# Performance work log

Measured on AMD Instinct MI355X. Metric: run time of the kernel, lower is better.

The kernel has to match this reference:

```python
import jax, jax.numpy as jnp
import numpy as np

N_NODES = 50000
N_EDGES = 800000
D_IN = 128
D_OUT = 128


def setup_inputs() -> dict:
    key = jax.random.key(0)
    k1, k2, k3, k4, k5 = jax.random.split(key, 5)
    x = jax.random.normal(k1, (N_NODES, D_IN), dtype=jnp.float32)
    edge_index = jax.random.randint(k2, (2, N_EDGES), 0, N_NODES, dtype=jnp.int64)
    # PyG SAGEConv params: lin_l (neighbors, with bias), lin_r (root, no bias)
    scale = 1.0 / np.sqrt(D_IN)
    W_l = jax.random.uniform(k3, (D_OUT, D_IN), dtype=jnp.float32, minval=-scale, maxval=scale)
    b_l = jax.random.uniform(k4, (D_OUT,), dtype=jnp.float32, minval=-scale, maxval=scale)
    W_r = jax.random.uniform(k5, (D_OUT, D_IN), dtype=jnp.float32, minval=-scale, maxval=scale)
    return {"x": x, "edge_index": edge_index, "W_l": W_l, "b_l": b_l, "W_r": W_r}


def reference(x, edge_index, W_l, b_l, W_r):
    src, dst = edge_index[0], edge_index[1]
    # mean aggregation of neighbor (source) features into destination nodes
    msg = x[src]  # [E, D_IN]
    agg_sum = jax.ops.segment_sum(msg, dst, num_segments=N_NODES)  # [N, D_IN]
    deg = jax.ops.segment_sum(jnp.ones((N_EDGES,), dtype=x.dtype), dst, num_segments=N_NODES)
    agg = agg_sum / jnp.maximum(deg, 1.0)[:, None]  # isolated nodes -> 0
    # out = lin_l(agg) + lin_r(x); ReLU from SAGE_NET wrapper (active=True)
    out = agg @ W_l.T + b_l + x @ W_r.T
    return jax.nn.relu(out)
```

## Files before the change

kernel.cpp:

```cpp
#include <hip/hip_runtime.h>
#include <hip/hip_bf16.h>

#define NNODES 50000
#define NEDGES 800000
#define DD 128
#define NPART 8
#define PSIZE 6250
#define CAP 64
#define NGROUPS 3910
#define WK_B (NGROUPS * 8 + 64)
#define WP2 68
#define ZROW ((u32)NNODES)

typedef unsigned int u32;
typedef unsigned short u16;
typedef short bf16x8 __attribute__((ext_vector_type(8)));
typedef float f32x4 __attribute__((ext_vector_type(4)));
typedef float f32x2 __attribute__((ext_vector_type(2)));

#if defined(__has_builtin)
#if __has_builtin(__builtin_amdgcn_cvt_pk_f32_fp8)
#define HAVE_HW_FP8 1
#endif
#endif

union U4B8 {
    uint4 u;
    bf16x8 b;
};

__device__ __forceinline__ u32 f2b(float f) {
    u32 u = __float_as_uint(f);
    u32 rounding = 0x7fffu + ((u >> 16) & 1u);
    return (u + rounding) >> 16;
}

__device__ __forceinline__ u32 f2e4m3(float f) {
    u32 u = __float_as_uint(f);
    u32 s = (u >> 31) << 7;
    u32 mag = u & 0x7fffffffu;
    if (mag < 0x3c800000u) return s;
    u32 t = mag + 0x0007FFFFu + ((mag >> 20) & 1u);
    u32 e = (t >> 23) - 120u;
    u32 m = (t >> 20) & 7u;
    if (e > 15u || (e == 15u && m == 7u)) { e = 15u; m = 6u; }
    return s | (e << 3) | m;
}

__device__ __forceinline__ void fp8x4_acc(u32 v, float& a0, float& a1,
                                          float& a2, float& a3) {
#ifdef HAVE_HW_FP8
    f32x2 lo = __builtin_amdgcn_cvt_pk_f32_fp8((int)v, false);
    f32x2 hi = __builtin_amdgcn_cvt_pk_f32_fp8((int)v, true);
    a0 += lo.x;
    a1 += lo.y;
    a2 += hi.x;
    a3 += hi.y;
#else
#pragma unroll
    for (int b = 0; b < 4; ++b) {
        u32 byte = (v >> (8 * b)) & 0xffu;
        u32 f = ((byte >> 7) << 31) | ((((byte >> 3) & 15u) + 120u) << 23) |
                ((byte & 7u) << 20);
        float val = (byte & 0x78u) ? __uint_as_float(f) : 0.f;
        if (b == 0) a0 += val;
        else if (b == 1) a1 += val;
        else if (b == 2) a2 += val;
        else a3 += val;
    }
#endif
}

__global__ __launch_bounds__(256) void work_k(
    const int* __restrict__ ei, u32* __restrict__ deg,
    u16* __restrict__ slots16, const float* __restrict__ x,
    u32* __restrict__ xb, u32* __restrict__ xq,
    const float* __restrict__ Wl, const float* __restrict__ Wr,
    u32* __restrict__ wb) {
    const int b = blockIdx.x, tid = threadIdx.x;
    if (b < NGROUPS * 8) {
        const u32 g = (u32)b >> 3, r8 = (u32)b & 7u;
        const u32 gm = g % 5u, gq = g / 5u;
        if (gm < 4u) {
            u32 fg = gq * 4u + gm;
            if (fg < 3125u) {
                u32 e = fg * 256u + tid;
                int dst = ei[NEDGES + e];
                if ((u32)(dst - r8 * PSIZE) < (u32)PSIZE) {
                    u32 pos = atomicAdd(deg + dst, 1u);
                    if (pos < CAP) slots16[(size_t)dst * CAP + pos] = (u16)ei[e];
                }
            }
        } else {
            u32 xi = gq * 8u + r8;
            if (xi < 6250u) {
                int i = (int)xi * 256 + tid;
                float4 v = ((const float4*)x)[i];
                uint2 o;
                o.x = f2b(v.x) | (f2b(v.y) << 16);
                o.y = f2b(v.z) | (f2b(v.w) << 16);
                ((uint2*)xb)[i] = o;
                xq[i] = f2e4m3(v.x) | (f2e4m3(v.y) << 8) | (f2e4m3(v.z) << 16) |
                        (f2e4m3(v.w) << 24);
            }
        }
    } else {
        int idx = (b - NGROUPS * 8) * 256 + tid;
        int o = idx >> 7, c = idx & 127, k0 = 2 * c;
        const float* src = (k0 < DD) ? (Wl + o * DD + k0) : (Wr + o * DD + (k0 - DD));
        wb[idx] = f2b(src[0]) | (f2b(src[1]) << 16);
        if (b == WK_B - 1 && tid < 32)
            xq[(size_t)ZROW * 32 + tid] = 0u;
    }
}

__global__ __launch_bounds__(256) void gather_k(
    const u32* __restrict__ xq, const u16* __restrict__ slots16,
    const u32* __restrict__ deg, u32* __restrict__ aggb) {
    u32 gid = blockIdx.x * 256u + threadIdx.x;
    u32 node = gid >> 6;
    u32 lane = gid & 63u;
    if (node >= NNODES) return;
    u32 d = deg[node];
    u32 cnt = min(d, (u32)CAP);
    u32 svp = (lane < cnt) ? (u32)slots16[(size_t)node * CAP + lane] : ZROW;
    const u32 half = lane >> 5;
    const u32 q = lane & 31u;
    float a0 = 0.f, a1 = 0.f, a2 = 0.f, a3 = 0.f;
    for (u32 j = 0; j < cnt; j += 16) {
        u32 v[8];
#pragma unroll
        for (int p = 0; p < 8; ++p) {
            u32 sA = __shfl(svp, (int)(j + 2 * p), 64);
            u32 sB = __shfl(svp, (int)(j + 2 * p + 1), 64);
            u32 s = half ? sB : sA;
            v[p] = xq[(size_t)s * 32 + q];
        }
#pragma unroll
        for (int p = 0; p < 8; ++p) fp8x4_acc(v[p], a0, a1, a2, a3);
    }
    a0 += __shfl_xor(a0, 32, 64);
    a1 += __shfl_xor(a1, 32, 64);
    a2 += __shfl_xor(a2, 32, 64);
    a3 += __shfl_xor(a3, 32, 64);
    if (lane < 32) {
        float inv = 1.0f / fmaxf((float)d, 1.0f);
        uint2 o;
        o.x = f2b(a0 * inv) | (f2b(a1 * inv) << 16);
        o.y = f2b(a2 * inv) | (f2b(a3 * inv) << 16);
        *(uint2*)&aggb[(size_t)node * 64 + q * 2] = o;
    }
}

__global__ __launch_bounds__(512, 4) void gemm_k(
    const u32* __restrict__ aggb, const u32* __restrict__ xb,
    const u32* __restrict__ wb, const float* __restrict__ bl,
    float* __restrict__ out) {
    __shared__ u32 w2[DD * WP2];
    __shared__ float sbias[DD];
    const int tid = threadIdx.x;
    const int row0 = blockIdx.x * 64;
    const int wave = tid >> 6, lane = tid & 63;
    const int m = lane & 15, quad = lane >> 4;
    const int rw = wave & 3;
    const int ch = wave >> 2;

    uint4 af_a[4], af_x[4];
    {
        int r = row0 + rw * 16 + m;
        r = r < NNODES ? r : NNODES - 1;
        const u32* arow = aggb + (size_t)r * 64;
        const u32* xrow = xb + (size_t)r * 64;
#pragma unroll
        for (int ks = 0; ks < 4; ++ks) {
            af_a[ks] = *(const uint4*)&arow[ks * 16 + quad * 4];
            af_x[ks] = *(const uint4*)&xrow[ks * 16 + quad * 4];
        }
    }

    for (int r = tid >> 5; r < DD; r += 16) {
        int c2 = (tid & 31) * 2;
        *(uint2*)&w2[r * WP2 + c2] = *(const uint2*)&wb[r * DD + c2];
    }
    if (tid < DD) sbias[tid] = bl[tid];
    __syncthreads();

    f32x4 acc[4];
#pragma unroll
    for (int nt = 0; nt < 4; ++nt) acc[nt] = (f32x4){0.f, 0.f, 0.f, 0.f};

#pragma unroll
    for (int ks = 0; ks < 4; ++ks) {
        U4B8 af;
        af.u = af_a[ks];
#pragma unroll
        for (int nt = 0; nt < 4; ++nt) {
            U4B8 bf;
            bf.u = *(const uint4*)&w2[((ch * 4 + nt) * 16 + m) * WP2 + ks * 16 +
                                      quad * 4];
            acc[nt] = __builtin_amdgcn_mfma_f32_16x16x32_bf16(af.b, bf.b,
                                                              acc[nt], 0, 0, 0);
        }
    }
    __syncthreads();
    for (int r = tid >> 5; r < DD; r += 16) {
        int c2 = (tid & 31) * 2;
        *(uint2*)&w2[r * WP2 + c2] = *(const uint2*)&wb[r * DD + 64 + c2];
    }
    __syncthreads();

#pragma unroll
    for (int ks = 0; ks < 4; ++ks) {
        U4B8 af;
        af.u = af_x[ks];
#pragma unroll
        for (int nt = 0; nt < 4; ++nt) {
            U4B8 bf;
            bf.u = *(const uint4*)&w2[((ch * 4 + nt) * 16 + m) * WP2 + ks * 16 +
                                      quad * 4];
            acc[nt] = __builtin_amdgcn_mfma_f32_16x16x32_bf16(af.b, bf.b,
                                                              acc[nt], 0, 0, 0);
        }
    }

#pragma unroll
    for (int nt = 0; nt < 4; ++nt) {
        int col = (ch * 4 + nt) * 16 + m;
        float b = sbias[col];
#pragma unroll
        for (int r_ = 0; r_ < 4; ++r_) {
            int row = row0 + rw * 16 + quad * 4 + r_;
            if (row < NNODES)
                out[(size_t)row * DD + col] = fmaxf(acc[nt][r_] + b, 0.f);
        }
    }
}

__global__ __launch_bounds__(256) void scatter_k(
    const float* __restrict__ x, const int* __restrict__ ei,
    float* __restrict__ agg, u32* __restrict__ deg) {
    u32 gid = blockIdx.x * 256u + threadIdx.x;
    u32 edge = gid >> 6;
    u32 lane = gid & 63u;
    if (edge >= NEDGES) return;
    int src = ei[edge];
    int dst = ei[NEDGES + edge];
    float2 v = ((const float2*)(x + (size_t)src * DD))[lane];
    float* p = agg + (size_t)dst * DD + lane * 2u;
    unsafeAtomicAdd(p, v.x);
    unsafeAtomicAdd(p + 1, v.y);
    if (lane == 0) atomicAdd(deg + dst, 1u);
}

__global__ __launch_bounds__(256) void mean_k(
    float* __restrict__ agg, const u32* __restrict__ deg) {
    u32 gid = blockIdx.x * 256u + threadIdx.x;
    u32 node = gid >> 6;
    u32 lane = gid & 63u;
    if (node >= NNODES) return;
    float inv = 1.0f / fmaxf((float)deg[node], 1.0f);
    float2* p = (float2*)(agg + (size_t)node * DD) + lane;
    float2 v = *p;
    *p = make_float2(v.x * inv, v.y * inv);
}

__global__ __launch_bounds__(256) void lin_l_k(
    float* __restrict__ agg,
    const float* __restrict__ Wl, const float* __restrict__ bl) {
    __shared__ u32 WT[DD * 65];
    __shared__ float rows[4 * DD];
    __shared__ float sbias[DD];
    const int tid = threadIdx.x;
    {
        u16* WTs = (u16*)WT;
        for (int i = tid; i < DD * DD; i += 256) {
            int o = i >> 7, k = i & 127;
            WTs[k * 130 + o] = (u16)f2b(Wl[i]);
        }
        if (tid < DD) sbias[tid] = bl[tid];
    }
    __syncthreads();
    const int h = tid & 63;
    const int nl = tid >> 6;
    for (int base = blockIdx.x * 4; base < NNODES; base += gridDim.x * 4) {
        ((float2*)rows)[tid] =
            ((const float2*)(agg + (size_t)(base + (tid >> 6)) * DD))[tid & 63];
        __syncthreads();
        float acc0 = sbias[2 * h], acc1 = sbias[2 * h + 1];
#pragma unroll
        for (int k = 0; k < DD; ++k) {
            float a = rows[nl * DD + k];
            u32 w2 = WT[k * 65 + h];
            acc0 = fmaf(a, __uint_as_float(w2 << 16), acc0);
            acc1 = fmaf(a, __uint_as_float(w2 & 0xffff0000u), acc1);
        }
        __syncthreads();
        ((float2*)(agg + (size_t)(base + nl) * DD))[h] = make_float2(acc0, acc1);
    }
}

__global__ __launch_bounds__(256) void lin_r_k(
    float* __restrict__ io, const float* __restrict__ x,
    const float* __restrict__ Wr) {
    __shared__ u32 WT[DD * 65];
    __shared__ float rows[4 * DD];
    const int tid = threadIdx.x;
    {
        u16* WTs = (u16*)WT;
        for (int i = tid; i < DD * DD; i += 256) {
            int o = i >> 7, k = i & 127;
            WTs[k * 130 + o] = (u16)f2b(Wr[i]);
        }
    }
    __syncthreads();
    const int h = tid & 63;
    const int nl = tid >> 6;
    for (int base = blockIdx.x * 4; base < NNODES; base += gridDim.x * 4) {
        ((float2*)rows)[tid] =
            ((const float2*)(x + (size_t)(base + (tid >> 6)) * DD))[tid & 63];
        __syncthreads();
        float2 t2 = ((const float2*)(io + (size_t)(base + nl) * DD))[h];
        float acc0 = t2.x, acc1 = t2.y;
#pragma unroll
        for (int k = 0; k < DD; ++k) {
            float a = rows[nl * DD + k];
            u32 w2 = WT[k * 65 + h];
            acc0 = fmaf(a, __uint_as_float(w2 << 16), acc0);
            acc1 = fmaf(a, __uint_as_float(w2 & 0xffff0000u), acc1);
        }
        acc0 = fmaxf(acc0, 0.f);
        acc1 = fmaxf(acc1, 0.f);
        __syncthreads();
        ((float2*)(io + (size_t)(base + nl) * DD))[h] = make_float2(acc0, acc1);
    }
}

extern "C" void kernel_launch(void* const* d_in, const int* in_sizes, int n_in,
                              void* d_out, int out_size, void* d_ws, size_t ws_size,
                              hipStream_t stream) {
    const float* x  = (const float*)d_in[0];
    const int*   ei = (const int*)d_in[1];
    const float* Wl = (const float*)d_in[2];
    const float* bl = (const float*)d_in[3];
    const float* Wr = (const float*)d_in[4];

    u32* deg     = (u32*)d_ws;
    u16* slots16 = (u16*)(deg + NNODES);
    u32* wb      = (u32*)d_ws + NNODES + (size_t)NNODES * (CAP / 2);
    u32* xb      = wb + 16384;
    u32* xq      = xb + (size_t)NNODES * 64;
    u32* aggb    = xq + (size_t)NNODES * 32 + 32;
    const size_t need =
        ((size_t)NNODES * (1 + CAP / 2 + 64 + 32 + 64) + 16384 + 32) * 4;

    if (ws_size >= need) {
        hipMemsetAsync(deg, 0, (size_t)NNODES * sizeof(u32), stream);
        work_k<<<WK_B, 256, 0, stream>>>(
            ei, deg, slots16, x, xb, xq, Wl, Wr, wb);
        gather_k<<<12500, 256, 0, stream>>>(xq, slots16, deg, aggb);
        gemm_k<<<(NNODES + 63) / 64, 512, 0, stream>>>(
            aggb, xb, wb, bl, (float*)d_out);
    } else {
        float* agg = (float*)d_out;
        hipMemsetAsync(d_out, 0, (size_t)NNODES * DD * sizeof(float), stream);
        hipMemsetAsync(d_ws, 0, (size_t)NNODES * sizeof(u32), stream);
        scatter_k<<<(NEDGES * 64) / 256, 256, 0, stream>>>(x, ei, agg, deg);
        mean_k<<<(NNODES * 64 + 255) / 256, 256, 0, stream>>>(agg, deg);
        lin_l_k<<<1024, 256, 0, stream>>>(agg, Wl, bl);
        lin_r_k<<<1024, 256, 0, stream>>>(agg, x, Wr);
    }
}
```

Before: 156.8 us.

## Build CSR slots with LDS-privatized counting per partition and edge slice

The edge-bucketing phase moves from one global atomic per edge to 64 blocks, each owning one of 8 destination partitions and one of 8 edge slices. Each block counts degrees in shared memory, reserves a contiguous range in global deg with one atomic per node, then fills slots using shared-memory atomics. This cuts global atomic traffic, at the cost of each block re-reading its edge slice twice and only 64 blocks doing the fill work. The x conversion and weight packing now run in 1024-thread blocks.

Result: slower. 170.1 us (+8.4%).

```diff
diff --git a/kernel.cpp b/kernel.cpp
--- a/kernel.cpp
+++ b/kernel.cpp
@@ -7,8 +7,10 @@
 #define NPART 8
 #define PSIZE 6250
 #define CAP 64
-#define NGROUPS 3910
-#define WK_B (NGROUPS * 8 + 64)
+#define FILL_B2 64
+#define XCV_B2 1563
+#define WPK_B2 16
+#define WKB2 (FILL_B2 + XCV_B2 + WPK_B2)
 #define WP2 68
 #define ZROW ((u32)NNODES)
 
@@ -71,45 +73,70 @@
 #endif
 }
 
-__global__ __launch_bounds__(256) void work_k(
+__global__ __launch_bounds__(1024) void work_k(
     const int* __restrict__ ei, u32* __restrict__ deg,
     u16* __restrict__ slots16, const float* __restrict__ x,
     u32* __restrict__ xb, u32* __restrict__ xq,
     const float* __restrict__ Wl, const float* __restrict__ Wr,
     u32* __restrict__ wb) {
+    __shared__ u32 cnt[PSIZE];
     const int b = blockIdx.x, tid = threadIdx.x;
-    if (b < NGROUPS * 8) {
-        const u32 g = (u32)b >> 3, r8 = (u32)b & 7u;
-        const u32 gm = g % 5u, gq = g / 5u;
-        if (gm < 4u) {
-            u32 fg = gq * 4u + gm;
-            if (fg < 3125u) {
-                u32 e = fg * 256u + tid;
-                int dst = ei[NEDGES + e];
-                if ((u32)(dst - r8 * PSIZE) < (u32)PSIZE) {
-                    u32 pos = atomicAdd(deg + dst, 1u);
-                    if (pos < CAP) slots16[(size_t)dst * CAP + pos] = (u16)ei[e];
-                }
+    if (b < FILL_B2) {
+        const u32 p = (u32)b & 7u, s = (u32)b >> 3;
+        const u32 base = p * PSIZE;
+        for (u32 i = tid; i < (u32)PSIZE; i += 1024u) cnt[i] = 0u;
+        __syncthreads();
+        const u32 T0 = s * 25000u;
+        for (u32 t4 = T0 + tid; t4 < T0 + 25000u; t4 += 1024u) {
+            uint4 dv = ((const uint4*)(ei + NEDGES))[t4];
+            if ((dv.x - base) < (u32)PSIZE) atomicAdd(&cnt[dv.x - base], 1u);
+            if ((dv.y - base) < (u32)PSIZE) atomicAdd(&cnt[dv.y - base], 1u);
+            if ((dv.z - base) < (u32)PSIZE) atomicAdd(&cnt[dv.z - base], 1u);
+            if ((dv.w - base) < (u32)PSIZE) atomicAdd(&cnt[dv.w - base], 1u);
+        }
+        __syncthreads();
+        for (u32 i = tid; i < (u32)PSIZE; i += 1024u) {
+            u32 c = cnt[i];
+            cnt[i] = c ? atomicAdd(deg + base + i, c) : 0u;
+        }
+        __syncthreads();
+        for (u32 t4 = T0 + tid; t4 < T0 + 25000u; t4 += 1024u) {
+            uint4 dv = ((const uint4*)(ei + NEDGES))[t4];
+            uint4 sv = ((const uint4*)ei)[t4];
+            if ((dv.x - base) < (u32)PSIZE) {
+                u32 pos = atomicAdd(&cnt[dv.x - base], 1u);
+                if (pos < CAP) slots16[(size_t)dv.x * CAP + pos] = (u16)sv.x;
             }
-        } else {
-            u32 xi = gq * 8u + r8;
-            if (xi < 6250u) {
-                int i = (int)xi * 256 + tid;
-                float4 v = ((const float4*)x)[i];
-                uint2 o;
-                o.x = f2b(v.x) | (f2b(v.y) << 16);
-                o.y = f2b(v.z) | (f2b(v.w) << 16);
-                ((uint2*)xb)[i] = o;
-                xq[i] = f2e4m3(v.x) | (f2e4m3(v.y) << 8) | (f2e4m3(v.z) << 16) |
-                        (f2e4m3(v.w) << 24);
+            if ((dv.y - base) < (u32)PSIZE) {
+                u32 pos = atomicAdd(&cnt[dv.y - base], 1u);
+                if (pos < CAP) slots16[(size_t)dv.y * CAP + pos] = (u16)sv.y;
             }
+            if ((dv.z - base) < (u32)PSIZE) {
+                u32 pos = atomicAdd(&cnt[dv.z - base], 1u);
+                if (pos < CAP) slots16[(size_t)dv.z * CAP + pos] = (u16)sv.z;
+            }
+            if ((dv.w - base) < (u32)PSIZE) {
+                u32 pos = atomicAdd(&cnt[dv.w - base], 1u);
+                if (pos < CAP) slots16[(size_t)dv.w * CAP + pos] = (u16)sv.w;
+            }
+        }
+    } else if (b < FILL_B2 + XCV_B2) {
+        int i = (b - FILL_B2) * 1024 + tid;
+        if (i < 1600000) {
+            float4 v = ((const float4*)x)[i];
+            uint2 o;
+            o.x = f2b(v.x) | (f2b(v.y) << 16);
+            o.y = f2b(v.z) | (f2b(v.w) << 16);
+            ((uint2*)xb)[i] = o;
+            xq[i] = f2e4m3(v.x) | (f2e4m3(v.y) << 8) | (f2e4m3(v.z) << 16) |
+                    (f2e4m3(v.w) << 24);
         }
     } else {
-        int idx = (b - NGROUPS * 8) * 256 + tid;
+        int idx = (b - FILL_B2 - XCV_B2) * 1024 + tid;
         int o = idx >> 7, c = idx & 127, k0 = 2 * c;
         const float* src = (k0 < DD) ? (Wl + o * DD + k0) : (Wr + o * DD + (k0 - DD));
         wb[idx] = f2b(src[0]) | (f2b(src[1]) << 16);
-        if (b == WK_B - 1 && tid < 32)
+        if (b == WKB2 - 1 && tid < 32)
             xq[(size_t)ZROW * 32 + tid] = 0u;
     }
 }
@@ -355,7 +382,7 @@
 
     if (ws_size >= need) {
         hipMemsetAsync(deg, 0, (size_t)NNODES * sizeof(u32), stream);
-        work_k<<<WK_B, 256, 0, stream>>>(
+        work_k<<<WKB2, 1024, 0, stream>>>(
             ei, deg, slots16, x, xb, xq, Wl, Wr, wb);
         gather_k<<<12500, 256, 0, stream>>>(xq, slots16, deg, aggb);
         gemm_k<<<(NNODES + 63) / 64, 512, 0, stream>>>(
```

## Replace global-atomic slot fill with two-pass bucket sort of edges by destination

Applied to the files above, without the earlier changes.

Edge placement into per-node slot lists now uses a counting sort. A histogram pass claims per-bucket offsets, a placement pass scatters packed (src,dst) pairs into a bucketed array, and a fill pass builds slots with shared-memory atomics per bucket. This is meant to replace the partitioned global atomicAdd on deg, which re-read the destination index array eight times. In exchange it adds two kernel launches, an extra 3.2 MB intermediate array, and only 64 blocks in the histogram and placement passes, which leaves most of the GPU idle. Slot order within a node becomes nondeterministic in a different way, and the 16-bit packing relies on node IDs fitting in 16 bits.

Measured after the change: 157.7 us. No clear change (+0.5%).

```diff
diff --git a/kernel.cpp b/kernel.cpp
--- a/kernel.cpp
+++ b/kernel.cpp
@@ -4,11 +4,13 @@
 #define NNODES 50000
 #define NEDGES 800000
 #define DD 128
-#define NPART 8
-#define PSIZE 6250
 #define CAP 64
-#define NGROUPS 3910
-#define WK_B (NGROUPS * 8 + 64)
+#define NSCAN 64
+#define NBKT 256
+#define BKTW 196
+#define XCV_B 6250
+#define WPK_B 64
+#define WKB3 (NSCAN + XCV_B + WPK_B)
 #define WP2 68
 #define ZROW ((u32)NNODES)
 
@@ -72,45 +74,108 @@
 }
 
 __global__ __launch_bounds__(256) void work_k(
-    const int* __restrict__ ei, u32* __restrict__ deg,
-    u16* __restrict__ slots16, const float* __restrict__ x,
+    const int* __restrict__ ei, u32* __restrict__ totals,
+    u32* __restrict__ claim, const float* __restrict__ x,
     u32* __restrict__ xb, u32* __restrict__ xq,
     const float* __restrict__ Wl, const float* __restrict__ Wr,
     u32* __restrict__ wb) {
+    __shared__ u32 hist[NBKT];
     const int b = blockIdx.x, tid = threadIdx.x;
-    if (b < NGROUPS * 8) {
-        const u32 g = (u32)b >> 3, r8 = (u32)b & 7u;
-        const u32 gm = g % 5u, gq = g / 5u;
-        if (gm < 4u) {
-            u32 fg = gq * 4u + gm;
-            if (fg < 3125u) {
-                u32 e = fg * 256u + tid;
-                int dst = ei[NEDGES + e];
-                if ((u32)(dst - r8 * PSIZE) < (u32)PSIZE) {
-                    u32 pos = atomicAdd(deg + dst, 1u);
-                    if (pos < CAP) slots16[(size_t)dst * CAP + pos] = (u16)ei[e];
-                }
-            }
-        } else {
-            u32 xi = gq * 8u + r8;
-            if (xi < 6250u) {
-                int i = (int)xi * 256 + tid;
-                float4 v = ((const float4*)x)[i];
-                uint2 o;
-                o.x = f2b(v.x) | (f2b(v.y) << 16);
-                o.y = f2b(v.z) | (f2b(v.w) << 16);
-                ((uint2*)xb)[i] = o;
-                xq[i] = f2e4m3(v.x) | (f2e4m3(v.y) << 8) | (f2e4m3(v.z) << 16) |
-                        (f2e4m3(v.w) << 24);
-            }
-        }
+    if (b < NSCAN) {
+        const u32 s = (u32)b;
+        if (tid < NBKT) hist[tid] = 0u;
+        __syncthreads();
+        const u32 T0 = s * 3125u, T1 = T0 + 3125u;
+        for (u32 t4 = T0 + tid; t4 < T1; t4 += 256u) {
+            uint4 dv = ((const uint4*)(ei + NEDGES))[t4];
+            atomicAdd(&hist[dv.x / BKTW], 1u);
+            atomicAdd(&hist[dv.y / BKTW], 1u);
+            atomicAdd(&hist[dv.z / BKTW], 1u);
+            atomicAdd(&hist[dv.w / BKTW], 1u);
+        }
+        __syncthreads();
+        if (tid < NBKT) {
+            u32 c = hist[tid];
+            claim[s * NBKT + tid] = c ? atomicAdd(&totals[tid], c) : 0u;
+        }
+    } else if (b < NSCAN + XCV_B) {
+        int i = (b - NSCAN) * 256 + tid;
+        float4 v = ((const float4*)x)[i];
+        uint2 o;
+        o.x = f2b(v.x) | (f2b(v.y) << 16);
+        o.y = f2b(v.z) | (f2b(v.w) << 16);
+        ((uint2*)xb)[i] = o;
+        xq[i] = f2e4m3(v.x) | (f2e4m3(v.y) << 8) | (f2e4m3(v.z) << 16) |
+                (f2e4m3(v.w) << 24);
     } else {
-        int idx = (b - NGROUPS * 8) * 256 + tid;
+        int idx = (b - NSCAN - XCV_B) * 256 + tid;
         int o = idx >> 7, c = idx & 127, k0 = 2 * c;
         const float* src = (k0 < DD) ? (Wl + o * DD + k0) : (Wr + o * DD + (k0 - DD));
         wb[idx] = f2b(src[0]) | (f2b(src[1]) << 16);
-        if (b == WK_B - 1 && tid < 32)
+        if (b == WKB3 - 1 && tid < 32)
             xq[(size_t)ZROW * 32 + tid] = 0u;
+    }
+}
+
+__global__ __launch_bounds__(256) void place_k(
+    const int* __restrict__ ei, const u32* __restrict__ totals,
+    const u32* __restrict__ claim, u32* __restrict__ sorted) {
+    __shared__ u32 tot[NBKT], base[NBKT], lcnt[NBKT];
+    const u32 s = blockIdx.x;
+    const int tid = threadIdx.x;
+    if (tid < NBKT) {
+        tot[tid] = totals[tid];
+        lcnt[tid] = 0u;
+    }
+    __syncthreads();
+    if (tid == 0) {
+        u32 acc = 0;
+        for (int i = 0; i < NBKT; ++i) { base[i] = acc; acc += tot[i]; }
+    }
+    __syncthreads();
+    const u32 T0 = s * 3125u, T1 = T0 + 3125u;
+    for (u32 t4 = T0 + tid; t4 < T1; t4 += 256u) {
+        uint4 dv = ((const uint4*)(ei + NEDGES))[t4];
+        uint4 sv = ((const uint4*)ei)[t4];
+#pragma unroll
+        for (int k = 0; k < 4; ++k) {
+            u32 d = k == 0 ? dv.x : k == 1 ? dv.y : k == 2 ? dv.z : dv.w;
+            u32 sr = k == 0 ? sv.x : k == 1 ? sv.y : k == 2 ? sv.z : sv.w;
+            u32 bk = d / BKTW;
+            u32 loc = atomicAdd(&lcnt[bk], 1u);
+            sorted[base[bk] + claim[s * NBKT + bk] + loc] = (sr << 16) | d;
+        }
+    }
+}
+
+__global__ __launch_bounds__(256) void fill2_k(
+    const u32* __restrict__ sorted, const u32* __restrict__ totals,
+    u32* __restrict__ deg, u16* __restrict__ slots16) {
+    __shared__ u32 cnt[BKTW];
+    __shared__ u32 sbase, stot;
+    const u32 g = blockIdx.x;
+    const int tid = threadIdx.x;
+    if (tid < BKTW) cnt[tid] = 0u;
+    if (tid == 0) {
+        u32 acc = 0;
+        for (u32 i = 0; i < g; ++i) acc += totals[i];
+        sbase = acc;
+        stot = totals[g];
+    }
+    __syncthreads();
+    const u32 E0 = sbase, E1 = sbase + stot;
+    const u32 nbase = g * BKTW;
+    for (u32 idx = E0 + tid; idx < E1; idx += 256u) {
+        u32 e = sorted[idx];
+        u32 d = e & 0xffffu;
+        u32 sr = e >> 16;
+        u32 pos = atomicAdd(&cnt[d - nbase], 1u);
+        if (pos < CAP) slots16[(size_t)d * CAP + pos] = (u16)sr;
+    }
+    __syncthreads();
+    for (u32 i = tid; i < (u32)BKTW; i += 256u) {
+        u32 node = nbase + i;
+        if (node < (u32)NNODES) deg[node] = cnt[i];
     }
 }
 
@@ -344,19 +409,25 @@
     const float* bl = (const float*)d_in[3];
     const float* Wr = (const float*)d_in[4];
 
-    u32* deg     = (u32*)d_ws;
+    u32* totals  = (u32*)d_ws;
+    u32* claim   = totals + NBKT;
+    u32* sorted  = claim + (size_t)NSCAN * NBKT;
+    u32* deg     = sorted + NEDGES;
     u16* slots16 = (u16*)(deg + NNODES);
-    u32* wb      = (u32*)d_ws + NNODES + (size_t)NNODES * (CAP / 2);
+    u32* wb      = deg + NNODES + (size_t)NNODES * (CAP / 2);
     u32* xb      = wb + 16384;
     u32* xq      = xb + (size_t)NNODES * 64;
     u32* aggb    = xq + (size_t)NNODES * 32 + 32;
     const size_t need =
-        ((size_t)NNODES * (1 + CAP / 2 + 64 + 32 + 64) + 16384 + 32) * 4;
+        ((size_t)NBKT + (size_t)NSCAN * NBKT + NEDGES +
+         (size_t)NNODES * (1 + CAP / 2 + 64 + 32 + 64) + 16384 + 32) * 4;
 
     if (ws_size >= need) {
-        hipMemsetAsync(deg, 0, (size_t)NNODES * sizeof(u32), stream);
-        work_k<<<WK_B, 256, 0, stream>>>(
-            ei, deg, slots16, x, xb, xq, Wl, Wr, wb);
+        hipMemsetAsync(totals, 0, NBKT * sizeof(u32), stream);
+        work_k<<<WKB3, 256, 0, stream>>>(
+            ei, totals, claim, x, xb, xq, Wl, Wr, wb);
+        place_k<<<NSCAN, 256, 0, stream>>>(ei, totals, claim, sorted);
+        fill2_k<<<NBKT, 256, 0, stream>>>(sorted, totals, deg, slots16);
         gather_k<<<12500, 256, 0, stream>>>(xq, slots16, deg, aggb);
         gemm_k<<<(NNODES + 63) / 64, 512, 0, stream>>>(
             aggb, xb, wb, bl, (float*)d_out);
```
